# Kernel optimization log

Hardware: AMD Instinct MI355X
Metric: run time of the kernel (lower is better)

## Reference

```python
import jax, jax.numpy as jnp
import numpy as np

B, T, D, H, DK, DV = 2, 2048, 1024, 16, 64, 64
_MASK_ADDER = -10000.0  # tf-models MaskedSoftmax convention


def setup_inputs() -> dict:
    key = jax.random.key(0)
    ks = jax.random.split(key, 8)
    s = 0.02
    return {
        "query": jax.random.normal(ks[0], (B, T, D), jnp.float32),
        "value": jax.random.normal(ks[1], (B, T, D), jnp.float32),
        "Wq": jax.random.normal(ks[2], (D, H, DK), jnp.float32) * s,
        "bq": jnp.zeros((H, DK), jnp.float32),
        "Wk": jax.random.normal(ks[3], (D, H, DK), jnp.float32) * s,
        "bk": jnp.zeros((H, DK), jnp.float32),
        "Wv": jax.random.normal(ks[4], (D, H, DV), jnp.float32) * s,
        "bv": jnp.zeros((H, DV), jnp.float32),
        "Wo": jax.random.normal(ks[5], (H, DV, D), jnp.float32) * s,
        "bo": jnp.zeros((D,), jnp.float32),
        "attention_mask": jnp.ones((B, T, T), jnp.int32),
    }


def reference(query, value, Wq, bq, Wk, bk, Wv, bv, Wo, bo, attention_mask):
    # key defaults to value (call() with key=None); training=False -> no dropout
    q = jnp.einsum("btd,dhk->bthk", query, Wq) + bq          # [B,T,H,DK]
    k = jnp.einsum("bsd,dhk->bshk", value, Wk) + bk          # [B,S,H,DK]
    v = jnp.einsum("bsd,dhk->bshk", value, Wv) + bv          # [B,S,H,DV]
    q = q * (1.0 / jnp.sqrt(jnp.asarray(DK, q.dtype)))
    scores = jnp.einsum("bthk,bshk->bhts", q, k)             # [B,H,T,S]
    # MaskedSoftmax: expand mask at axis 1, additive -10000 on masked slots
    adder = (1.0 - attention_mask.astype(scores.dtype))[:, None, :, :] * _MASK_ADDER
    probs = jax.nn.softmax(scores + adder, axis=-1)
    ctx = jnp.einsum("bhts,bshv->bthv", probs, v)            # [B,T,H,DV]
    out = jnp.einsum("bthv,hvd->btd", ctx, Wo) + bo          # [B,T,D]
    return out
```

## Files before the change

### kernel.cpp

```cpp
#include <hip/hip_runtime.h>
#include <hip/hip_bf16.h>
#include <stdint.h>

#define TSEQ 2048
#define DMODEL 1024
#define NHEAD 16
#define HDIM 64
#define MROWS 4096
#define L2E 1.44269504088896340736f

typedef unsigned short u16;
typedef __attribute__((ext_vector_type(8))) short bf16x8;
typedef __attribute__((ext_vector_type(8))) unsigned short u16x8;
typedef __attribute__((ext_vector_type(4))) unsigned short u16x4;
typedef __attribute__((ext_vector_type(4))) float f32x4;

__device__ inline u16 f2bf(float f) {
  __hip_bfloat16 h(f);
  return __builtin_bit_cast(u16, h);
}

__device__ inline float fexp2(float x) { float r; asm("v_exp_f32 %0, %1" : "=v"(r) : "v"(x)); return r; }

__device__ inline unsigned cvtpk_bf16(float a, float b) {
  unsigned r; asm("v_cvt_pk_bf16_f32 %0, %1, %2" : "=v"(r) : "v"(a), "v"(b)); return r;
}

__device__ inline void gload16(const void* g, void* l) {
  __builtin_amdgcn_global_load_lds((const __attribute__((address_space(1))) void*)g,
                                   (__attribute__((address_space(3))) void*)l, 16, 0, 0);
}

__global__ void cvt2(const float* __restrict__ q, const float* __restrict__ v,
                     u16* __restrict__ qo, u16* __restrict__ vo) {
  const float* in = blockIdx.y ? v : q;
  u16* out = blockIdx.y ? vo : qo;
  int i = (blockIdx.x * blockDim.x + threadIdx.x) * 4;
  float4 x = *(const float4*)(in + i);
  u16x4 o;
  o.x = f2bf(x.x); o.y = f2bf(x.y); o.z = f2bf(x.z); o.w = f2bf(x.w);
  *(u16x4*)(out + i) = o;
}

__global__ void wtrans4(const float* __restrict__ Wq, const float* __restrict__ Wk,
                        const float* __restrict__ Wv, const float* __restrict__ Wo,
                        u16* __restrict__ WT3, u16* __restrict__ WoT) {
  __shared__ float tile[32][33];
  const int z = blockIdx.z;
  const float* W = z == 0 ? Wq : z == 1 ? Wk : z == 2 ? Wv : Wo;
  u16* WT = z < 3 ? (WT3 + (size_t)z * 1024 * 1024) : WoT;
  const int bx = blockIdx.x, by = blockIdx.y;
  const int tr = threadIdx.x >> 3;
  const int tc4 = (threadIdx.x & 7) * 4;
  float4 v = *(const float4*)(W + (size_t)(by * 32 + tr) * 1024 + bx * 32 + tc4);
  tile[tr][tc4 + 0] = v.x; tile[tr][tc4 + 1] = v.y;
  tile[tr][tc4 + 2] = v.z; tile[tr][tc4 + 3] = v.w;
  __syncthreads();
  u16x4 o;
  o.x = f2bf(tile[tc4 + 0][tr]); o.y = f2bf(tile[tc4 + 1][tr]);
  o.z = f2bf(tile[tc4 + 2][tr]); o.w = f2bf(tile[tc4 + 3][tr]);
  *(u16x4*)(WT + (size_t)(bx * 32 + tr) * 1024 + by * 32 + tc4) = o;
}

__global__ void maskflag(const int* __restrict__ mask, int* __restrict__ flags) {
  const int st = blockIdx.x, qt = blockIdx.y, b = blockIdx.z;
  const int row = qt * 128 + (threadIdx.x >> 1);
  const int col0 = st * 128 + (threadIdx.x & 1) * 64;
  const int* p = mask + (size_t)b * TSEQ * TSEQ + (size_t)row * TSEQ + col0;
  int ok = 1;
  #pragma unroll
  for (int j = 0; j < 64; j += 4) {
    int4 v = *(const int4*)(p + j);
    ok &= (v.x == 1) & (v.y == 1) & (v.z == 1) & (v.w == 1);
  }
  ok = __all(ok);
  __shared__ int s[4];
  if ((threadIdx.x & 63) == 0) s[threadIdx.x >> 6] = ok;
  __syncthreads();
  if (threadIdx.x == 0) flags[(b * 16 + qt) * 16 + st] = s[0] & s[1] & s[2] & s[3];
}

__global__ void vtrans(const u16* __restrict__ V, u16* __restrict__ VT) {
  __shared__ u16 tile[64][72];
  const int bh = blockIdx.y;
  const int t0 = blockIdx.x * 64;
  const u16* src = V + ((size_t)bh * TSEQ + t0) * 64;
  const int r = threadIdx.x >> 3, sg = threadIdx.x & 7;
  #pragma unroll
  for (int i = 0; i < 2; ++i) {
    int row = r + i * 32;
    u16x8 v = *(const u16x8*)(src + (size_t)row * 64 + sg * 8);
    #pragma unroll
    for (int j = 0; j < 8; ++j) tile[row][sg * 8 + j] = v[j];
  }
  __syncthreads();
  u16* dst = VT + (size_t)bh * 64 * TSEQ;
  #pragma unroll
  for (int i = 0; i < 2; ++i) {
    int v = r + i * 32;
    u16x8 o;
    #pragma unroll
    for (int j = 0; j < 8; ++j) o[j] = tile[sg * 8 + j][v];
    *(u16x8*)(dst + (size_t)v * TSEQ + t0 + sg * 8) = o;
  }
}

__global__ __launch_bounds__(256) void gemm_qkv(
    const u16* __restrict__ qxb, const u16* __restrict__ vxb, const u16* __restrict__ WT3,
    const float* __restrict__ bq, const float* __restrict__ bk, const float* __restrict__ bv,
    u16* __restrict__ Qb, u16* __restrict__ Kb, u16* __restrict__ Vb, float qscale) {
  __shared__ u16 As[128 * 64];
  __shared__ u16 Bs[128 * 64];
  const int tid = threadIdx.x;
  const int w = tid >> 6, lane = tid & 63;
  const int lo = lane & 15, hi = lane >> 4;
  const int m0 = blockIdx.x * 128, n0 = blockIdx.y * 128;
  const int nsel = n0 >> 10;
  const u16* A = nsel == 0 ? qxb : vxb;
  const float* bias = nsel == 0 ? bq : nsel == 1 ? bk : bv;
  u16* dst = nsel == 0 ? Qb : nsel == 1 ? Kb : Vb;
  const float scl = nsel == 0 ? qscale : 1.0f;
  const int wm = (w >> 1) * 64, wn = (w & 1) * 64;
  f32x4 acc[4][4] = {};
  const int loff = w * 4096 + lane * 16;
  for (int kt = 0; kt < 16; ++kt) {
    #pragma unroll
    for (int i = 0; i < 4; ++i) {
      const int off = loff + i * 1024;
      const int row = off >> 7;
      const int g = ((off >> 4) & 7) ^ (row & 7);
      gload16(A + (size_t)(m0 + row) * 1024 + kt * 64 + g * 8, (char*)As + off);
      gload16(WT3 + (size_t)(n0 + row) * 1024 + kt * 64 + g * 8, (char*)Bs + off);
    }
    __syncthreads();
    #pragma unroll
    for (int kk = 0; kk < 2; ++kk) {
      bf16x8 af[4], bfr[4];
      #pragma unroll
      for (int mi = 0; mi < 4; ++mi) {
        int row = wm + mi * 16 + lo;
        af[mi] = *(const bf16x8*)(As + row * 64 + (((kk * 4 + hi) ^ (row & 7)) << 3));
      }
      #pragma unroll
      for (int ni = 0; ni < 4; ++ni) {
        int row = wn + ni * 16 + lo;
        bfr[ni] = *(const bf16x8*)(Bs + row * 64 + (((kk * 4 + hi) ^ (row & 7)) << 3));
      }
      #pragma unroll
      for (int mi = 0; mi < 4; ++mi)
        #pragma unroll
        for (int ni = 0; ni < 4; ++ni)
          acc[mi][ni] = __builtin_amdgcn_mfma_f32_16x16x32_bf16(af[mi], bfr[ni], acc[mi][ni], 0, 0, 0);
    }
    __syncthreads();
  }
  #pragma unroll
  for (int ni = 0; ni < 4; ++ni) {
    const int col = (n0 + wn + ni * 16 + lo) & 1023;
    const float bc = bias[col];
    #pragma unroll
    for (int mi = 0; mi < 4; ++mi) {
      #pragma unroll
      for (int r = 0; r < 4; ++r) {
        const int row = m0 + wm + mi * 16 + hi * 4 + r;
        const float v = (acc[mi][ni][r] + bc) * scl;
        dst[(size_t)(((row >> 11) * NHEAD + (col >> 6)) * TSEQ + (row & 2047)) * HDIM + (col & 63)] = f2bf(v);
      }
    }
  }
}

__global__ __launch_bounds__(256) void gemm_o(const u16* __restrict__ A, const u16* __restrict__ BT,
                                              const float* __restrict__ bias, float* __restrict__ C) {
  __shared__ u16 As[64 * 64];
  __shared__ u16 Bs[128 * 64];
  const int tid = threadIdx.x;
  const int w = tid >> 6, lane = tid & 63;
  const int lo = lane & 15, hi = lane >> 4;
  const int m0 = blockIdx.x * 64, n0 = blockIdx.y * 128;
  const int wm = (w >> 1) * 32, wn = (w & 1) * 64;
  f32x4 acc[2][4] = {};
  for (int kt = 0; kt < 16; ++kt) {
    #pragma unroll
    for (int i = 0; i < 2; ++i) {
      const int off = tid * 16 + i * 4096;
      const int row = off >> 7;
      const int g = ((off >> 4) & 7) ^ (row & 7);
      gload16(A + (size_t)(m0 + row) * 1024 + kt * 64 + g * 8, (char*)As + off);
    }
    #pragma unroll
    for (int i = 0; i < 4; ++i) {
      const int off = tid * 16 + i * 4096;
      const int row = off >> 7;
      const int g = ((off >> 4) & 7) ^ (row & 7);
      gload16(BT + (size_t)(n0 + row) * 1024 + kt * 64 + g * 8, (char*)Bs + off);
    }
    __syncthreads();
    #pragma unroll
    for (int kk = 0; kk < 2; ++kk) {
      bf16x8 af[2], bfr[4];
      #pragma unroll
      for (int mi = 0; mi < 2; ++mi) {
        int row = wm + mi * 16 + lo;
        af[mi] = *(const bf16x8*)(As + row * 64 + (((kk * 4 + hi) ^ (row & 7)) << 3));
      }
      #pragma unroll
      for (int ni = 0; ni < 4; ++ni) {
        int row = wn + ni * 16 + lo;
        bfr[ni] = *(const bf16x8*)(Bs + row * 64 + (((kk * 4 + hi) ^ (row & 7)) << 3));
      }
      #pragma unroll
      for (int mi = 0; mi < 2; ++mi)
        #pragma unroll
        for (int ni = 0; ni < 4; ++ni)
          acc[mi][ni] = __builtin_amdgcn_mfma_f32_16x16x32_bf16(af[mi], bfr[ni], acc[mi][ni], 0, 0, 0);
    }
    __syncthreads();
  }
  #pragma unroll
  for (int ni = 0; ni < 4; ++ni) {
    const int col = n0 + wn + ni * 16 + lo;
    const float bc = bias[col];
    #pragma unroll
    for (int mi = 0; mi < 2; ++mi)
      #pragma unroll
      for (int r = 0; r < 4; ++r) {
        const int row = m0 + wm + mi * 16 + hi * 4 + r;
        C[(size_t)row * DMODEL + col] = acc[mi][ni][r] + bc;
      }
  }
}

__global__ __launch_bounds__(256) void flash(
    const u16* __restrict__ Q, const u16* __restrict__ K, const u16* __restrict__ VT,
    const int* __restrict__ mask, const int* __restrict__ flags, u16* __restrict__ ctx) {
  __shared__ u16 Ks[2][64 * 64];
  __shared__ u16 Vs[2][64 * 64];
  __shared__ u16 Ps[4][32 * 64];
  const int tid = threadIdx.x, w = tid >> 6, lane = tid & 63;
  const int lo = lane & 15, hi = lane >> 4;
  const int qt = blockIdx.x, bh = blockIdx.y;
  const int b = bh >> 4, h = bh & 15;
  const int q0 = qt * 128;
  u16* Pw = &Ps[w][0];

  const int soff = w * 2048 + lane * 16;
  const int srow0 = w * 16 + (lane >> 3);
  const int g8 = (((lane & 7) ^ (lane >> 3)) << 3);

  bf16x8 qf[2][2];
  #pragma unroll
  for (int mi = 0; mi < 2; ++mi)
    #pragma unroll
    for (int kk = 0; kk < 2; ++kk)
      qf[mi][kk] = *(const bf16x8*)(Q + ((size_t)bh * TSEQ + q0 + w * 32 + mi * 16 + lo) * 64 + kk * 32 + hi * 8);

  unsigned fl = 0;
  {
    const int* fp = flags + (b * 16 + qt) * 16;
    #pragma unroll
    for (int i = 0; i < 4; ++i) {
      int4 v = *(const int4*)(fp + i * 4);
      fl |= (unsigned)((v.x & 1) | ((v.y & 1) << 1) | ((v.z & 1) << 2) | ((v.w & 1) << 3)) << (4 * i);
    }
  }

  f32x4 o[2][4] = {};
  float mrow[2] = {-1e30f, -1e30f}, lrow[2] = {0.f, 0.f};

#define STAGE(buf, st_) do {                                                         \
    const u16* kb_ = K + ((size_t)bh * TSEQ + (st_) * 64) * 64;                      \
    const u16* vb_ = VT + (size_t)bh * 64 * TSEQ + (st_) * 64;                       \
    gload16(kb_ + (size_t)srow0 * 64 + g8, (char*)Ks[buf] + soff);                   \
    gload16(kb_ + (size_t)(srow0 + 8) * 64 + g8, (char*)Ks[buf] + soff + 1024);      \
    gload16(vb_ + (size_t)srow0 * TSEQ + g8, (char*)Vs[buf] + soff);                 \
    gload16(vb_ + (size_t)(srow0 + 8) * TSEQ + g8, (char*)Vs[buf] + soff + 1024);    \
  } while (0)

  int cur = 0;
  STAGE(0, 0);
  __syncthreads();

  for (int st = 0; st < 32; ++st) {
    if (st < 31) STAGE(cur ^ 1, st + 1);
    const u16* Ksb = Ks[cur];
    const u16* Vsb = Vs[cur];

    f32x4 sc[2][4] = {};
    __builtin_amdgcn_s_setprio(1);
    #pragma unroll
    for (int kk = 0; kk < 2; ++kk) {
      const int p = ((kk * 4 + hi) ^ (lo & 7)) << 3;
      #pragma unroll
      for (int si = 0; si < 4; ++si) {
        bf16x8 kf = *(const bf16x8*)(Ksb + (si * 16 + lo) * 64 + p);
        #pragma unroll
        for (int mi = 0; mi < 2; ++mi)
          sc[mi][si] = __builtin_amdgcn_mfma_f32_16x16x32_bf16(kf, qf[mi][kk], sc[mi][si], 0, 0, 0);
      }
    }
    __builtin_amdgcn_s_setprio(0);

    if (!((fl >> (st >> 1)) & 1)) {
      #pragma unroll
      for (int mi = 0; mi < 2; ++mi) {
        const int t = q0 + w * 32 + mi * 16 + lo;
        #pragma unroll
        for (int si = 0; si < 4; ++si)
          #pragma unroll
          for (int r = 0; r < 4; ++r) {
            int s = st * 64 + si * 16 + hi * 4 + r;
            int mv = mask[(size_t)b * TSEQ * TSEQ + (size_t)t * TSEQ + s];
            sc[mi][si][r] += (1.0f - (float)mv) * -14426.950408f;
          }
      }
    }

    float pm[2];
    #pragma unroll
    for (int mi = 0; mi < 2; ++mi) {
      float m = sc[mi][0][0];
      #pragma unroll
      for (int si = 0; si < 4; ++si)
        #pragma unroll
        for (int r = 0; r < 4; ++r) m = fmaxf(m, sc[mi][si][r]);
      m = fmaxf(m, __shfl_xor(m, 16));
      m = fmaxf(m, __shfl_xor(m, 32));
      pm[mi] = m;
    }

    if (__any(fmaxf(pm[0] - mrow[0], pm[1] - mrow[1]) > 11.0f)) {
      #pragma unroll
      for (int mi = 0; mi < 2; ++mi) {
        float mn = fmaxf(mrow[mi], pm[mi]);
        float a = fexp2(mrow[mi] - mn);
        lrow[mi] *= a;
        mrow[mi] = mn;
        #pragma unroll
        for (int r = 0; r < 4; ++r) {
          float ar = __shfl(a, hi * 4 + r);
          #pragma unroll
          for (int vj = 0; vj < 4; ++vj) o[mi][vj][r] *= ar;
        }
      }
    }

    #pragma unroll
    for (int mi = 0; mi < 2; ++mi) {
      float rs = 0.f;
      const int tl = mi * 16 + lo;
      #pragma unroll
      for (int si = 0; si < 4; ++si) {
        float p0 = fexp2(sc[mi][si][0] - mrow[mi]);
        float p1 = fexp2(sc[mi][si][1] - mrow[mi]);
        float p2 = fexp2(sc[mi][si][2] - mrow[mi]);
        float p3 = fexp2(sc[mi][si][3] - mrow[mi]);
        rs += (p0 + p1) + (p2 + p3);
        unsigned w0 = cvtpk_bf16(p0, p1);
        unsigned w1 = cvtpk_bf16(p2, p3);
        const int seg = si * 2 + (hi >> 1);
        *(uint2*)((char*)Pw + tl * 128 + ((seg ^ (lo & 7)) << 4) + ((hi & 1) << 3)) = make_uint2(w0, w1);
      }
      rs += __shfl_xor(rs, 16);
      rs += __shfl_xor(rs, 32);
      lrow[mi] += rs;
    }

    __builtin_amdgcn_s_setprio(1);
    #pragma unroll
    for (int kk = 0; kk < 2; ++kk) {
      const int p = ((kk * 4 + hi) ^ (lo & 7)) << 3;
      bf16x8 pa[2];
      #pragma unroll
      for (int mi = 0; mi < 2; ++mi)
        pa[mi] = *(const bf16x8*)(Pw + (mi * 16 + lo) * 64 + p);
      #pragma unroll
      for (int vj = 0; vj < 4; ++vj) {
        bf16x8 vf = *(const bf16x8*)(Vsb + (vj * 16 + lo) * 64 + p);
        #pragma unroll
        for (int mi = 0; mi < 2; ++mi)
          o[mi][vj] = __builtin_amdgcn_mfma_f32_16x16x32_bf16(pa[mi], vf, o[mi][vj], 0, 0, 0);
      }
    }
    __builtin_amdgcn_s_setprio(0);

    __syncthreads();
    cur ^= 1;
  }
#undef STAGE

  #pragma unroll
  for (int mi = 0; mi < 2; ++mi) {
    const float inv = 1.0f / lrow[mi];
    #pragma unroll
    for (int r = 0; r < 4; ++r) {
      const float ir = __shfl(inv, hi * 4 + r);
      const int t = q0 + w * 32 + mi * 16 + hi * 4 + r;
      #pragma unroll
      for (int vj = 0; vj < 4; ++vj) {
        const int col = h * 64 + vj * 16 + lo;
        ctx[(size_t)(b * TSEQ + t) * DMODEL + col] = f2bf(o[mi][vj][r] * ir);
      }
    }
  }
}

extern "C" void kernel_launch(void* const* d_in, const int* in_sizes, int n_in,
                              void* d_out, int out_size, void* d_ws, size_t ws_size,
                              hipStream_t stream) {
  (void)in_sizes; (void)n_in; (void)out_size; (void)ws_size;
  const float* query = (const float*)d_in[0];
  const float* value = (const float*)d_in[1];
  const float* Wq = (const float*)d_in[2];
  const float* bq = (const float*)d_in[3];
  const float* Wk = (const float*)d_in[4];
  const float* bk = (const float*)d_in[5];
  const float* Wv = (const float*)d_in[6];
  const float* bv = (const float*)d_in[7];
  const float* Wo = (const float*)d_in[8];
  const float* bo = (const float*)d_in[9];
  const int* amask = (const int*)d_in[10];

  char* ws = (char*)d_ws;
  const size_t MB = 1 << 20;
  u16* qxb = (u16*)(ws + 0 * MB);
  u16* vxb = (u16*)(ws + 8 * MB);
  u16* WT3 = (u16*)(ws + 16 * MB);
  u16* WoT = (u16*)(ws + 22 * MB);
  u16* Qb  = (u16*)(ws + 24 * MB);
  u16* Kb  = (u16*)(ws + 32 * MB);
  u16* Vb  = (u16*)(ws + 40 * MB);
  u16* VTb = (u16*)(ws + 48 * MB);
  u16* ctx = (u16*)(ws + 56 * MB);
  int* flg = (int*)(ws + 64 * MB);

  cvt2<<<dim3(4096, 2), 256, 0, stream>>>(query, value, qxb, vxb);
  wtrans4<<<dim3(32, 32, 4), 256, 0, stream>>>(Wq, Wk, Wv, Wo, WT3, WoT);
  maskflag<<<dim3(16, 16, 2), 256, 0, stream>>>(amask, flg);

  gemm_qkv<<<dim3(32, 24), 256, 0, stream>>>(qxb, vxb, WT3, bq, bk, bv, Qb, Kb, Vb, 0.125f * L2E);
  vtrans<<<dim3(32, 32), 256, 0, stream>>>(Vb, VTb);
  flash<<<dim3(16, 32), 256, 0, stream>>>(Qb, Kb, VTb, amask, flg, ctx);
  gemm_o<<<dim3(64, 8), 256, 0, stream>>>(ctx, WoT, bo, (float*)d_out);
}
```

Before: 152.7 us.

## Split flash attention over two KV halves and merge with a combine kernel

Splits the attention KV loop into two halves, run as separate blocks along a new grid dimension. The original grid of 512 blocks gets doubled so more of the GPU's compute units stay busy. Each half writes unnormalised bf16 partial outputs plus its row max and sum, and a new combine kernel rescales and merges them into ctx. The cost is an extra launch, extra global traffic for the partial outputs, and bf16 rounding of the unnormalised partials. It also reuses workspace regions for the qx and V buffers, which are no longer needed at that point.

```diff
diff --git a/kernel.cpp b/kernel.cpp
--- a/kernel.cpp
+++ b/kernel.cpp
@@ -18,6 +18,9 @@
 __device__ inline u16 f2bf(float f) {
   __hip_bfloat16 h(f);
   return __builtin_bit_cast(u16, h);
+}
+__device__ inline float bf2f(u16 x) {
+  return __builtin_bit_cast(float, ((unsigned)x) << 16);
 }
 
 __device__ inline float fexp2(float x) { float r; asm("v_exp_f32 %0, %1" : "=v"(r) : "v"(x)); return r; }
@@ -231,17 +234,19 @@
   }
 }
 
-__global__ __launch_bounds__(256) void flash(
+__global__ __launch_bounds__(256) void flash_part(
     const u16* __restrict__ Q, const u16* __restrict__ K, const u16* __restrict__ VT,
-    const int* __restrict__ mask, const int* __restrict__ flags, u16* __restrict__ ctx) {
+    const int* __restrict__ mask, const int* __restrict__ flags,
+    u16* __restrict__ Op, float2* __restrict__ ml) {
   __shared__ u16 Ks[2][64 * 64];
   __shared__ u16 Vs[2][64 * 64];
   __shared__ u16 Ps[4][32 * 64];
   const int tid = threadIdx.x, w = tid >> 6, lane = tid & 63;
   const int lo = lane & 15, hi = lane >> 4;
-  const int qt = blockIdx.x, bh = blockIdx.y;
-  const int b = bh >> 4, h = bh & 15;
+  const int qt = blockIdx.x, bh = blockIdx.y, kvh = blockIdx.z;
+  const int b = bh >> 4;
   const int q0 = qt * 128;
+  const int st0 = kvh * 16;
   u16* Pw = &Ps[w][0];
 
   const int soff = w * 2048 + lane * 16;
@@ -278,11 +283,12 @@
   } while (0)
 
   int cur = 0;
-  STAGE(0, 0);
+  STAGE(0, st0);
   __syncthreads();
 
-  for (int st = 0; st < 32; ++st) {
-    if (st < 31) STAGE(cur ^ 1, st + 1);
+  for (int it = 0; it < 16; ++it) {
+    const int st = st0 + it;
+    if (it < 15) STAGE(cur ^ 1, st + 1);
     const u16* Ksb = Ks[cur];
     const u16* Vsb = Vs[cur];
 
@@ -389,20 +395,43 @@
   }
 #undef STAGE
 
+  const size_t rbase = (size_t)kvh * 65536 + (size_t)bh * TSEQ;
   #pragma unroll
   for (int mi = 0; mi < 2; ++mi) {
-    const float inv = 1.0f / lrow[mi];
+    const int trow = q0 + w * 32 + mi * 16;
+    if (hi == 0)
+      ml[rbase + trow + lo] = make_float2(mrow[mi], lrow[mi]);
     #pragma unroll
     for (int r = 0; r < 4; ++r) {
-      const float ir = __shfl(inv, hi * 4 + r);
-      const int t = q0 + w * 32 + mi * 16 + hi * 4 + r;
-      #pragma unroll
-      for (int vj = 0; vj < 4; ++vj) {
-        const int col = h * 64 + vj * 16 + lo;
-        ctx[(size_t)(b * TSEQ + t) * DMODEL + col] = f2bf(o[mi][vj][r] * ir);
-      }
-    }
-  }
+      const int t = trow + hi * 4 + r;
+      #pragma unroll
+      for (int vj = 0; vj < 4; ++vj)
+        Op[(rbase + t) * 64 + vj * 16 + lo] = f2bf(o[mi][vj][r]);
+    }
+  }
+}
+
+__global__ __launch_bounds__(256) void combine(const u16* __restrict__ Op,
+                                               const float2* __restrict__ ml,
+                                               u16* __restrict__ ctx) {
+  const int tid = threadIdx.x;
+  const int row = blockIdx.x * 16 + (tid >> 4);
+  const int c4 = (tid & 15) * 4;
+  const float2 A = ml[row];
+  const float2 B = ml[65536 + row];
+  const float m = fmaxf(A.x, B.x);
+  float eA = fexp2(A.x - m), eB = fexp2(B.x - m);
+  const float inv = 1.0f / (A.y * eA + B.y * eB);
+  eA *= inv; eB *= inv;
+  u16x4 oa = *(const u16x4*)(Op + (size_t)row * 64 + c4);
+  u16x4 ob = *(const u16x4*)(Op + ((size_t)65536 + row) * 64 + c4);
+  float v0 = bf2f(oa.x) * eA + bf2f(ob.x) * eB;
+  float v1 = bf2f(oa.y) * eA + bf2f(ob.y) * eB;
+  float v2 = bf2f(oa.z) * eA + bf2f(ob.z) * eB;
+  float v3 = bf2f(oa.w) * eA + bf2f(ob.w) * eB;
+  uint2 pw = make_uint2(cvtpk_bf16(v0, v1), cvtpk_bf16(v2, v3));
+  const int b = row >> 15, h = (row >> 11) & 15, t = row & 2047;
+  *(uint2*)(ctx + ((size_t)(b * TSEQ + t)) * DMODEL + h * 64 + c4) = pw;
 }
 
 extern "C" void kernel_launch(void* const* d_in, const int* in_sizes, int n_in,
@@ -433,6 +462,8 @@
   u16* VTb = (u16*)(ws + 48 * MB);
   u16* ctx = (u16*)(ws + 56 * MB);
   int* flg = (int*)(ws + 64 * MB);
+  u16* Op    = (u16*)(ws + 0 * MB);
+  float2* ml = (float2*)(ws + 40 * MB);
 
   cvt2<<<dim3(4096, 2), 256, 0, stream>>>(query, value, qxb, vxb);
   wtrans4<<<dim3(32, 32, 4), 256, 0, stream>>>(Wq, Wk, Wv, Wo, WT3, WoT);
@@ -440,6 +471,7 @@
 
   gemm_qkv<<<dim3(32, 24), 256, 0, stream>>>(qxb, vxb, WT3, bq, bk, bv, Qb, Kb, Vb, 0.125f * L2E);
   vtrans<<<dim3(32, 32), 256, 0, stream>>>(Vb, VTb);
-  flash<<<dim3(16, 32), 256, 0, stream>>>(Qb, Kb, VTb, amask, flg, ctx);
+  flash_part<<<dim3(16, 32, 2), 256, 0, stream>>>(Qb, Kb, VTb, amask, flg, Op, ml);
+  combine<<<4096, 256, 0, stream>>>(Op, ml, ctx);
   gemm_o<<<dim3(64, 8), 256, 0, stream>>>(ctx, WoT, bo, (float*)d_out);
 }
```

Result: slower. 161.0 us (+5.4%).
